# Performance work log

Hardware: AMD Instinct MI355X
Metric: run time of the kernel (lower is better)

## Reference

```python
import jax, jax.numpy as jnp
import numpy as np

SEQ, B, V, E, H, L, S_SRC = 128, 32, 32000, 1024, 1024, 3, 64


def setup_inputs() -> dict:
    key = jax.random.key(0)
    ks = jax.random.split(key, 8)
    sc = 0.05
    return {
        "tokens": jax.random.randint(ks[0], (SEQ, B), 0, V),
        "emb_W": jax.random.normal(ks[1], (V, E), jnp.float32) * 0.1,
        "W_ih": jax.random.normal(ks[2], (L, 4 * H, E), jnp.float32) * sc,
        "W_hh": jax.random.normal(ks[3], (L, 4 * H, H), jnp.float32) * sc,
        "b_ih": jnp.zeros((L, 4 * H), jnp.float32),
        "b_hh": jnp.zeros((L, 4 * H), jnp.float32),
        "attn_Win": jax.random.normal(ks[4], (E, E), jnp.float32) * sc,
        "attn_Wout": jax.random.normal(ks[5], (E, 2 * E), jnp.float32) * sc,
        "final_b": jnp.zeros((V,), jnp.float32),
        "encoder_outs": jax.random.normal(ks[6], (S_SRC, B, E), jnp.float32),
        "h0": jnp.zeros((L, B, H), jnp.float32),
        "c0": jnp.zeros((L, B, H), jnp.float32),
    }


def reference(tokens, emb_W, W_ih, W_hh, b_ih, b_hh, attn_Win, attn_Wout,
              final_b, encoder_outs, h0, c0):
    # Eval mode: all dropouts (dropoute/i/h/out) are identity.
    emb = emb_W[tokens]                                  # [SEQ, B, E]
    ctx = jnp.transpose(encoder_outs, (1, 0, 2))         # [B, S_src, E]

    def lstm_cell(x, h, c, l):
        gates = x @ W_ih[l].T + b_ih[l] + h @ W_hh[l].T + b_hh[l]  # [B, 4H]
        i, f, g, o = jnp.split(gates, 4, axis=-1)        # torch order: i,f,g,o
        i, f, o = jax.nn.sigmoid(i), jax.nn.sigmoid(f), jax.nn.sigmoid(o)
        g = jnp.tanh(g)
        c_new = f * c + i * g
        return o * jnp.tanh(c_new), c_new

    def step(carry, x_t):
        h, c = carry                                     # each [L, B, H]
        hs, cs = [], []
        inp = x_t
        for l in range(L):
            h_new, c_new = lstm_cell(inp, h[l], c[l], l)
            hs.append(h_new)
            cs.append(c_new)
            inp = h_new                                  # dropouth is identity
        # SoftDotAttention on last layer hidden
        target = h_new @ attn_Win.T                      # [B, E]
        attn = jax.nn.softmax(jnp.einsum('bse,be->bs', ctx, target), axis=-1)
        wc = jnp.einsum('bs,bse->be', attn, ctx)         # weighted context
        h_tilde = jnp.tanh(jnp.concatenate([wc, h_new], axis=-1) @ attn_Wout.T)
        return (jnp.stack(hs), jnp.stack(cs)), h_tilde

    (_, _), outs = jax.lax.scan(step, (h0, c0), emb)     # outs: [SEQ, B, E]
    logits = outs @ emb_W.T + final_b                    # tied weights: [SEQ, B, V]
    return logits
```

## Files before the change

### kernel.cpp

```cpp
#include <hip/hip_runtime.h>
#include <cstdint>
#include <cstddef>

#define SEQ   128
#define BB    32
#define EE    1024
#define HH    1024
#define G4    4096
#define VV    32000
#define NROWS 4096

typedef _Float16 h16x8 __attribute__((ext_vector_type(8)));
typedef _Float16 h16x4 __attribute__((ext_vector_type(4)));
typedef float f32x4  __attribute__((ext_vector_type(4)));

#define AS_G(p) ((const __attribute__((address_space(1))) void*)(p))
#define AS_L(p) ((__attribute__((address_space(3))) void*)(p))

__device__ __forceinline__ float sigmf(float x) { return 1.0f / (1.0f + expf(-x)); }

#define OFF_SYNC    0ull
#define OFF_HFRAG   40960ull
#define OFF_EMB     434176ull
#define OFF_X0      8822784ull
#define OFF_WIH0    42377216ull
#define OFF_WP4     50765824ull
#define OFF_WP0     84320256ull
#define OFF_EMBW    92708864ull
#define OFF_WIN     158244864ull
#define OFF_WOUT    160342016ull
#define OFF_ENC     164536320ull
#define OFF_H2ALL   168730624ull
#define OFF_CONCAT  177119232ull
#define OFF_TARGET  193896448ull
#define OFF_HT      202285056ull
#define WS_NEEDED   210673664ull

__global__ __launch_bounds__(256) void k_conv(const float* __restrict__ s,
                                              _Float16* __restrict__ d, int n4) {
  int i = blockIdx.x * blockDim.x + threadIdx.x;
  int st = gridDim.x * blockDim.x;
  for (; i < n4; i += st) {
    float4 v = ((const float4*)s)[i];
    h16x4 o; o[0] = (_Float16)v.x; o[1] = (_Float16)v.y; o[2] = (_Float16)v.z; o[3] = (_Float16)v.w;
    ((h16x4*)d)[i] = o;
  }
}

__global__ __launch_bounds__(256) void k_gather(const int* __restrict__ tok,
                                                const float* __restrict__ embW,
                                                _Float16* __restrict__ emb) {
  int row = blockIdx.x;
  int t = tok[row];
  float4 v = ((const float4*)(embW + (size_t)t * EE))[threadIdx.x];
  h16x4 o; o[0] = (_Float16)v.x; o[1] = (_Float16)v.y; o[2] = (_Float16)v.z; o[3] = (_Float16)v.w;
  ((h16x4*)(emb + (size_t)row * EE))[threadIdx.x] = o;
}

__global__ __launch_bounds__(256) void k_packw4(const float* __restrict__ Wih,
                                                const float* __restrict__ Whh,
                                                _Float16* __restrict__ out) {
  int i = blockIdx.x * blockDim.x + threadIdx.x;
  int st = gridDim.x * blockDim.x;
  const int total = 256 * 65536;
  for (; i < total; i += st) {
    int w = i >> 16, rem = i & 65535;
    int mat = rem >> 14, jj = (rem >> 10) & 15, k = rem & 1023;
    int layer = 1 + (mat >> 1), isHH = mat & 1;
    int row = ((jj >> 2) << 10) + (w << 2) + (jj & 3);
    int ks = k ^ ((jj & 7) << 3);
    const float* src = (isHH ? Whh : Wih) + (size_t)layer * G4 * 1024 + (size_t)row * 1024 + ks;
    out[i] = (_Float16)(*src);
  }
}

__global__ __launch_bounds__(256) void k_packw0(const float* __restrict__ Whh,
                                                _Float16* __restrict__ out) {
  int i = blockIdx.x * blockDim.x + threadIdx.x;
  int st = gridDim.x * blockDim.x;
  const int total = 256 * 16384;
  for (; i < total; i += st) {
    int w = i >> 14, rem = i & 16383;
    int ks = rem >> 9, lane = (rem >> 3) & 63, e = rem & 7;
    int jj = lane & 15, q = lane >> 4;
    int row = ((jj >> 2) << 10) + (w << 2) + (jj & 3);
    int k = ks * 32 + q * 8 + e;
    out[i] = (_Float16)Whh[(size_t)row * 1024 + k];
  }
}

__global__ __launch_bounds__(256) void k_init(const float* __restrict__ h0,
                                              _Float16* __restrict__ hfrag,
                                              unsigned* __restrict__ sync) {
  int i = blockIdx.x * blockDim.x + threadIdx.x;
  if (i < 64 + 8192) sync[i] = 0u;
  if (i >= 3 * BB * HH) return;
  int l = i >> 15, rem = i & 32767;
  int b = rem >> 10, n = rem & 1023;
  int parI = (l == 1) ? 0 : 1;
  int tbb = b >> 4, ks = n >> 5, q = (n >> 3) & 3, e = n & 7;
  int lane2 = (b & 15) | (q << 4);
  hfrag[(size_t)(l * 2 + parI) * 32768 + ((size_t)(tbb * 32 + ks) * 64 + lane2) * 8 + e] =
      (_Float16)h0[i];
}

template <int EPI>
__global__ __launch_bounds__(256) void k_gemm(const _Float16* __restrict__ A,
                                              const _Float16* __restrict__ B,
                                              void* __restrict__ C, int M, int N, int K,
                                              const float* __restrict__ bias1,
                                              const float* __restrict__ bias2) {
  __shared__ _Float16 As[2][128 * 32];
  __shared__ _Float16 Bs[2][128 * 32];
  const int ntn = N / 128;
  const int nwg = gridDim.x;
  const int bid = (blockIdx.x & 7) * (nwg >> 3) + (blockIdx.x >> 3);
  const int tm = bid / ntn, tn = bid % ntn;
  const int tid = threadIdx.x, lane = tid & 63;
  const int wv = tid >> 6, wr = wv >> 1, wc = wv & 1;
  f32x4 acc[4][4] = {};

  auto stage = [&](int buf, int k0) {
#pragma unroll
    for (int i = 0; i < 2; ++i) {
      int eo = (i * 256 + tid) * 8;
      int r = eo >> 5, c = eo & 31;
      __builtin_amdgcn_global_load_lds(AS_G(A + (size_t)(tm * 128 + r) * K + k0 + c),
                                       AS_L(&As[buf][eo]), 16, 0, 0);
      __builtin_amdgcn_global_load_lds(AS_G(B + (size_t)(tn * 128 + r) * K + k0 + c),
                                       AS_L(&Bs[buf][eo]), 16, 0, 0);
    }
  };
  stage(0, 0);
  __syncthreads();
  const int nk = K / 32;
  for (int kt = 0; kt < nk; ++kt) {
    if (kt + 1 < nk) stage((kt + 1) & 1, (kt + 1) * 32);
    const int buf = kt & 1;
    h16x8 af[4], bfr[4];
#pragma unroll
    for (int mi = 0; mi < 4; ++mi)
      af[mi] = *(const h16x8*)&As[buf][(wr * 64 + mi * 16 + (lane & 15)) * 32 + (lane >> 4) * 8];
#pragma unroll
    for (int ni = 0; ni < 4; ++ni)
      bfr[ni] = *(const h16x8*)&Bs[buf][(wc * 64 + ni * 16 + (lane & 15)) * 32 + (lane >> 4) * 8];
#pragma unroll
    for (int mi = 0; mi < 4; ++mi)
#pragma unroll
      for (int ni = 0; ni < 4; ++ni)
        acc[mi][ni] = __builtin_amdgcn_mfma_f32_16x16x32_f16(af[mi], bfr[ni], acc[mi][ni], 0, 0, 0);
    __syncthreads();
  }
  const int rbase = tm * 128 + wr * 64;
  const int cbase = tn * 128 + wc * 64;
#pragma unroll
  for (int mi = 0; mi < 4; ++mi) {
#pragma unroll
    for (int ni = 0; ni < 4; ++ni) {
#pragma unroll
      for (int r = 0; r < 4; ++r) {
        int mm = rbase + mi * 16 + (lane >> 4) * 4 + r;
        int nn = cbase + ni * 16 + (lane & 15);
        float v = acc[mi][ni][r];
        if (EPI == 0) {
          ((float*)C)[(size_t)mm * N + nn] = v + bias1[nn];
        } else if (EPI == 1) {
          ((_Float16*)C)[(size_t)mm * N + nn] = (_Float16)v;
        } else if (EPI == 2) {
          ((_Float16*)C)[(size_t)mm * N + nn] = (_Float16)tanhf(v);
        } else {
          ((_Float16*)C)[(size_t)mm * N + nn] = (_Float16)(v + bias1[nn] + bias2[nn]);
        }
      }
    }
  }
}

__global__ __launch_bounds__(512) void k_recur(const _Float16* __restrict__ Wp4,
                                               const _Float16* __restrict__ Wp0,
                                               const _Float16* __restrict__ X0bf,
                                               _Float16* __restrict__ hfrag,
                                               _Float16* __restrict__ h2all,
                                               _Float16* __restrict__ concat,
                                               const float* __restrict__ bih,
                                               const float* __restrict__ bhh,
                                               const float* __restrict__ c0p,
                                               unsigned* __restrict__ sync) {
  extern __shared__ char lds[];
  _Float16* ldsW = (_Float16*)lds;
  float* redbuf = (float*)(lds + 131072);
  _Float16* hstage = (_Float16*)(lds + 131072);
  float* gbuf = (float*)(lds + 149504);
  unsigned* arrive = sync + 64;

  const int w = blockIdx.x;
  const int tid = threadIdx.x, lane = tid & 63, wv = tid >> 6;
  const int tb = wv & 1, kq = wv >> 1;
  const int row = (lane >> 4) * 4, col = lane & 15;

  for (int i = 0; i < 16; ++i) {
    int eo = (i * 512 + tid) * 8;
    *(h16x8*)&ldsW[eo] = *(const h16x8*)(Wp4 + (size_t)w * 65536 + eo);
  }
  h16x8 w0reg[8];
#pragma unroll
  for (int i = 0; i < 8; ++i)
    w0reg[i] = *(const h16x8*)(Wp0 + (size_t)w * 16384 + ((size_t)(kq * 8 + i) * 64 + lane) * 8);

  const int eb = tid >> 2, eni = tid & 3, en = w * 4 + eni;
  float c0r = 0.f, c1r = 0.f, c2r = 0.f;
  float b1r[4] = {0, 0, 0, 0}, b2r[4] = {0, 0, 0, 0};
  if (tid < 128) {
    c0r = c0p[0 * BB * HH + eb * HH + en];
    c1r = c0p[1 * BB * HH + eb * HH + en];
    c2r = c0p[2 * BB * HH + eb * HH + en];
#pragma unroll
    for (int g = 0; g < 4; ++g) {
      b1r[g] = bih[1 * G4 + g * 1024 + en] + bhh[1 * G4 + g * 1024 + en];
      b2r[g] = bih[2 * G4 + g * 1024 + en] + bhh[2 * G4 + g * 1024 + en];
    }
  }
  const int pk_l = tid >> 5, pk_r = tid & 31;
  const size_t pk_idx = ((size_t)(((pk_r >> 4) * 32 + (w >> 3)) * 64 + (pk_r & 15) +
                                  (((w >> 1) & 3) << 4))) * 8 + 4 * (w & 1);
  __syncthreads();

  for (int tau = 0; tau < 130; ++tau) {
    const int p = tau & 1;
    const _Float16* h0r = hfrag + (size_t)(0 + (1 - p)) * 32768;
    const _Float16* h1r = hfrag + (size_t)(2 + (1 - p)) * 32768;
    const _Float16* h2r = hfrag + (size_t)(4 + (1 - p)) * 32768;

    h16x8 a0[8], a1[8], a2[8];
#pragma unroll
    for (int i = 0; i < 8; ++i) {
      int ks = kq * 8 + i;
      size_t off = ((size_t)(tb * 32 + ks) * 64 + lane) * 8;
      a0[i] = *(const h16x8*)(h0r + off);
      a1[i] = *(const h16x8*)(h1r + off);
      a2[i] = *(const h16x8*)(h2r + off);
    }
    float xg0 = 0.f, xg1 = 0.f, xg2 = 0.f, xg3 = 0.f;
    if (tid < 128 && tau < 128) {
      size_t xb = ((size_t)(tau * BB + eb)) * G4 + en;
      xg0 = (float)X0bf[xb];        xg1 = (float)X0bf[xb + 1024];
      xg2 = (float)X0bf[xb + 2048]; xg3 = (float)X0bf[xb + 3072];
    }
    f32x4 acc0 = {}, acc1 = {}, acc2 = {};
#pragma unroll
    for (int i = 0; i < 8; ++i) {
      int ks = kq * 8 + i;
      int jj = lane & 15, q = lane >> 4;
      int kk = (ks * 32 + q * 8) ^ ((jj & 7) << 3);
      const h16x8 bw1i = *(const h16x8*)&ldsW[0 * 16384 + jj * 1024 + kk];
      const h16x8 bw1h = *(const h16x8*)&ldsW[1 * 16384 + jj * 1024 + kk];
      const h16x8 bw2i = *(const h16x8*)&ldsW[2 * 16384 + jj * 1024 + kk];
      const h16x8 bw2h = *(const h16x8*)&ldsW[3 * 16384 + jj * 1024 + kk];
      acc0 = __builtin_amdgcn_mfma_f32_16x16x32_f16(a0[i], w0reg[i], acc0, 0, 0, 0);
      acc1 = __builtin_amdgcn_mfma_f32_16x16x32_f16(a0[i], bw1i, acc1, 0, 0, 0);
      acc1 = __builtin_amdgcn_mfma_f32_16x16x32_f16(a1[i], bw1h, acc1, 0, 0, 0);
      acc2 = __builtin_amdgcn_mfma_f32_16x16x32_f16(a1[i], bw2i, acc2, 0, 0, 0);
      acc2 = __builtin_amdgcn_mfma_f32_16x16x32_f16(a2[i], bw2h, acc2, 0, 0, 0);
    }
    if (kq >= 1) {
      int s = kq - 1;
#pragma unroll
      for (int r = 0; r < 4; ++r) {
        redbuf[((0 * 3 + s) * 2 + tb) * 256 + (row + r) * 16 + col] = acc0[r];
        redbuf[((1 * 3 + s) * 2 + tb) * 256 + (row + r) * 16 + col] = acc1[r];
        redbuf[((2 * 3 + s) * 2 + tb) * 256 + (row + r) * 16 + col] = acc2[r];
      }
    }
    __syncthreads();
    if (kq == 0) {
#pragma unroll
      for (int r = 0; r < 4; ++r) {
        float v0 = acc0[r], v1 = acc1[r], v2 = acc2[r];
#pragma unroll
        for (int s = 0; s < 3; ++s) {
          v0 += redbuf[((0 * 3 + s) * 2 + tb) * 256 + (row + r) * 16 + col];
          v1 += redbuf[((1 * 3 + s) * 2 + tb) * 256 + (row + r) * 16 + col];
          v2 += redbuf[((2 * 3 + s) * 2 + tb) * 256 + (row + r) * 16 + col];
        }
        gbuf[(0 * 32 + tb * 16 + row + r) * 16 + col] = v0;
        gbuf[(1 * 32 + tb * 16 + row + r) * 16 + col] = v1;
        gbuf[(2 * 32 + tb * 16 + row + r) * 16 + col] = v2;
      }
    }
    __syncthreads();
    if (tid < 128) {
      if (tau < 128) {
        float gi = gbuf[(0 * 32 + eb) * 16 + eni] + xg0;
        float gf = gbuf[(0 * 32 + eb) * 16 + 4 + eni] + xg1;
        float gg = gbuf[(0 * 32 + eb) * 16 + 8 + eni] + xg2;
        float go = gbuf[(0 * 32 + eb) * 16 + 12 + eni] + xg3;
        c0r = sigmf(gf) * c0r + sigmf(gi) * tanhf(gg);
        hstage[0 * 128 + tid] = (_Float16)(sigmf(go) * tanhf(c0r));
      }
      if (tau >= 1 && tau < 129) {
        float gi = gbuf[(1 * 32 + eb) * 16 + eni] + b1r[0];
        float gf = gbuf[(1 * 32 + eb) * 16 + 4 + eni] + b1r[1];
        float gg = gbuf[(1 * 32 + eb) * 16 + 8 + eni] + b1r[2];
        float go = gbuf[(1 * 32 + eb) * 16 + 12 + eni] + b1r[3];
        c1r = sigmf(gf) * c1r + sigmf(gi) * tanhf(gg);
        hstage[1 * 128 + tid] = (_Float16)(sigmf(go) * tanhf(c1r));
      }
      if (tau >= 2) {
        float gi = gbuf[(2 * 32 + eb) * 16 + eni] + b2r[0];
        float gf = gbuf[(2 * 32 + eb) * 16 + 4 + eni] + b2r[1];
        float gg = gbuf[(2 * 32 + eb) * 16 + 8 + eni] + b2r[2];
        float go = gbuf[(2 * 32 + eb) * 16 + 12 + eni] + b2r[3];
        c2r = sigmf(gf) * c2r + sigmf(gi) * tanhf(gg);
        float h = sigmf(go) * tanhf(c2r);
        _Float16 hb = (_Float16)h;
        hstage[2 * 128 + tid] = hb;
        int t2 = tau - 2;
        h2all[(size_t)(t2 * BB + eb) * HH + en] = hb;
        concat[(size_t)(t2 * BB + eb) * 2048 + 1024 + en] = hb;
      }
    }
    __syncthreads();
    {
      bool act = (tid < 96) &&
                 ((pk_l == 0) ? (tau < 128)
                  : (pk_l == 1) ? (tau >= 1 && tau < 129) : (tau >= 2));
      if (act) {
        unsigned long long v = *(const unsigned long long*)&hstage[pk_l * 128 + pk_r * 4];
        __hip_atomic_store(
            (unsigned long long*)(hfrag + (size_t)(pk_l * 2 + p) * 32768 + pk_idx), v,
            __ATOMIC_RELAXED, __HIP_MEMORY_SCOPE_AGENT);
      }
      asm volatile("s_waitcnt vmcnt(0)" ::: "memory");
    }
    __syncthreads();
    if (tid == 0)
      __hip_atomic_store(&arrive[w * 32], (unsigned)(tau + 1), __ATOMIC_RELAXED,
                         __HIP_MEMORY_SCOPE_AGENT);
    if (tau < 129) {
      if (tid < 64) {
        for (;;) {
          bool ok = true;
#pragma unroll
          for (int j = 0; j < 4; ++j) {
            unsigned v = __hip_atomic_load(&arrive[(tid * 4 + j) * 32], __ATOMIC_RELAXED,
                                           __HIP_MEMORY_SCOPE_AGENT);
            ok &= (v >= (unsigned)(tau + 1));
          }
          if (__all(ok)) break;
          __builtin_amdgcn_s_sleep(1);
        }
        __builtin_amdgcn_fence(__ATOMIC_ACQUIRE, "agent");
      }
      __syncthreads();
    }
  }
}

__global__ __launch_bounds__(256) void k_attn(const _Float16* __restrict__ target,
                                              const _Float16* __restrict__ encb,
                                              _Float16* __restrict__ concat) {
  __shared__ float sc[64];
  __shared__ float att[64];
  int m = blockIdx.x, b = m & 31;
  int tid = threadIdx.x, lane = tid & 63, wv = tid >> 6;
  const h16x8* tp = (const h16x8*)(target + (size_t)m * EE + lane * 16);
  h16x8 tg0 = tp[0], tg1 = tp[1];
  for (int si = 0; si < 16; ++si) {
    int s = wv * 16 + si;
    const h16x8* ep = (const h16x8*)(encb + ((size_t)s * BB + b) * EE + lane * 16);
    h16x8 e0 = ep[0], e1 = ep[1];
    float a = 0.f;
#pragma unroll
    for (int j = 0; j < 8; ++j) a += (float)e0[j] * (float)tg0[j];
#pragma unroll
    for (int j = 0; j < 8; ++j) a += (float)e1[j] * (float)tg1[j];
#pragma unroll
    for (int off = 32; off >= 1; off >>= 1) a += __shfl_xor(a, off);
    if (lane == 0) sc[s] = a;
  }
  __syncthreads();
  if (wv == 0) {
    float v = sc[lane], mx = v;
#pragma unroll
    for (int off = 32; off >= 1; off >>= 1) mx = fmaxf(mx, __shfl_xor(mx, off));
    float e = expf(v - mx), sm = e;
#pragma unroll
    for (int off = 32; off >= 1; off >>= 1) sm += __shfl_xor(sm, off);
    att[lane] = e / sm;
  }
  __syncthreads();
  int e4 = tid * 4;
  float a0 = 0, a1 = 0, a2 = 0, a3 = 0;
  for (int s = 0; s < 64; ++s) {
    float wgt = att[s];
    h16x4 ev = *(const h16x4*)(encb + ((size_t)s * BB + b) * EE + e4);
    a0 += wgt * (float)ev[0]; a1 += wgt * (float)ev[1];
    a2 += wgt * (float)ev[2]; a3 += wgt * (float)ev[3];
  }
  h16x4 o; o[0] = (_Float16)a0; o[1] = (_Float16)a1; o[2] = (_Float16)a2; o[3] = (_Float16)a3;
  *(h16x4*)(concat + (size_t)m * 2048 + e4) = o;
}

extern "C" void kernel_launch(void* const* d_in, const int* in_sizes, int n_in,
                              void* d_out, int out_size, void* d_ws, size_t ws_size,
                              hipStream_t stream) {
  const int* tokens = (const int*)d_in[0];
  const float* embW = (const float*)d_in[1];
  const float* Wih = (const float*)d_in[2];
  const float* Whh = (const float*)d_in[3];
  const float* bih = (const float*)d_in[4];
  const float* bhh = (const float*)d_in[5];
  const float* Win = (const float*)d_in[6];
  const float* Wout = (const float*)d_in[7];
  const float* finalb = (const float*)d_in[8];
  const float* enc = (const float*)d_in[9];
  const float* h0 = (const float*)d_in[10];
  const float* c0 = (const float*)d_in[11];
  (void)in_sizes; (void)n_in; (void)out_size;
  if (ws_size < WS_NEEDED) return;

  char* ws = (char*)d_ws;
  unsigned* sync = (unsigned*)(ws + OFF_SYNC);
  _Float16* hfrag = (_Float16*)(ws + OFF_HFRAG);
  _Float16* emb = (_Float16*)(ws + OFF_EMB);
  _Float16* X0bf = (_Float16*)(ws + OFF_X0);
  _Float16* Wih0b = (_Float16*)(ws + OFF_WIH0);
  _Float16* Wp4 = (_Float16*)(ws + OFF_WP4);
  _Float16* Wp0 = (_Float16*)(ws + OFF_WP0);
  _Float16* embWb = (_Float16*)(ws + OFF_EMBW);
  _Float16* Winb = (_Float16*)(ws + OFF_WIN);
  _Float16* Woutb = (_Float16*)(ws + OFF_WOUT);
  _Float16* encb = (_Float16*)(ws + OFF_ENC);
  _Float16* h2all = (_Float16*)(ws + OFF_H2ALL);
  _Float16* concat = (_Float16*)(ws + OFF_CONCAT);
  _Float16* target = (_Float16*)(ws + OFF_TARGET);
  _Float16* ht = (_Float16*)(ws + OFF_HT);

  const unsigned LDSB = 155648;
  static int lds_set = 0;
  if (!lds_set) {
    hipFuncSetAttribute((const void*)k_recur, hipFuncAttributeMaxDynamicSharedMemorySize,
                        (int)LDSB);
    lds_set = 1;
  }

  k_conv<<<4096, 256, 0, stream>>>(embW, embWb, VV * EE / 4);
  k_conv<<<1024, 256, 0, stream>>>(Wih, Wih0b, G4 * EE / 4);
  k_conv<<<512, 256, 0, stream>>>(Win, Winb, EE * EE / 4);
  k_conv<<<512, 256, 0, stream>>>(Wout, Woutb, EE * 2048 / 4);
  k_conv<<<512, 256, 0, stream>>>(enc, encb, 64 * BB * EE / 4);
  k_gather<<<NROWS, 256, 0, stream>>>(tokens, embW, emb);
  k_packw4<<<8192, 256, 0, stream>>>(Wih, Whh, Wp4);
  k_packw0<<<4096, 256, 0, stream>>>(Whh, Wp0);
  k_init<<<384, 256, 0, stream>>>(h0, hfrag, sync);

  k_gemm<3><<<32 * 32, 256, 0, stream>>>(emb, Wih0b, X0bf, NROWS, G4, EE, bih, bhh);

  k_recur<<<256, 512, LDSB, stream>>>(Wp4, Wp0, X0bf, hfrag, h2all, concat,
                                      bih, bhh, c0, sync);

  k_gemm<1><<<32 * 8, 256, 0, stream>>>(h2all, Winb, target, NROWS, EE, EE, nullptr, nullptr);
  k_attn<<<NROWS, 256, 0, stream>>>(target, encb, concat);
  k_gemm<2><<<32 * 8, 256, 0, stream>>>(concat, Woutb, ht, NROWS, EE, 2048, nullptr, nullptr);

  k_gemm<0><<<32 * 250, 256, 0, stream>>>(ht, embWb, d_out, NROWS, VV, EE, finalb, nullptr);
}
```

Before: 1.697 ms.

## Add 256x256-tile triple-buffered GEMM for input projection and vocab logits

Adds a new GEMM kernel with 256x256 output tiles, 512 threads, three-stage global-to-LDS async loads and wave priority boosting around the MFMA block. It is used for the layer-0 input projection and the large tied-embedding logits GEMM, replacing the 128x128 kernel, to raise data reuse per loaded tile and overlap loads with compute. The old kernel keeps only the fp16 and tanh epilogues. The new kernel uses more registers and LDS per workgroup, so occupancy is lower. It also adds a blockIdx remap across groups of eight.

```diff
diff --git a/kernel.cpp b/kernel.cpp
--- a/kernel.cpp
+++ b/kernel.cpp
@@ -162,12 +162,100 @@
         int mm = rbase + mi * 16 + (lane >> 4) * 4 + r;
         int nn = cbase + ni * 16 + (lane & 15);
         float v = acc[mi][ni][r];
+        if (EPI == 1) {
+          ((_Float16*)C)[(size_t)mm * N + nn] = (_Float16)v;
+        } else {
+          ((_Float16*)C)[(size_t)mm * N + nn] = (_Float16)tanhf(v);
+        }
+      }
+    }
+  }
+}
+
+template <int EPI>
+__global__ __launch_bounds__(512, 2) void k_gemm256(const _Float16* __restrict__ A,
+                                                    const _Float16* __restrict__ B,
+                                                    void* __restrict__ C, int M, int N, int K,
+                                                    const float* __restrict__ bias1,
+                                                    const float* __restrict__ bias2) {
+  extern __shared__ char glds[];
+  _Float16* Asl = (_Float16*)glds;
+  _Float16* Bsl = (_Float16*)(glds + 3 * 8192 * 2);
+  const int ntn = N / 256;
+  const int nwg = gridDim.x;
+  const int bid = (blockIdx.x & 7) * (nwg >> 3) + (blockIdx.x >> 3);
+  const int tm = bid / ntn, tn = bid % ntn;
+  const int tid = threadIdx.x, lane = tid & 63;
+  const int wid = tid >> 6, wm = wid >> 2, wn = wid & 3;
+  const int fr = lane & 15, fc = lane >> 4;
+  const int srow0 = tid >> 2, sg = tid & 3;
+
+  f32x4 acc[8][4] = {};
+  const int nt = K / 32;
+
+  auto stage = [&](int t) {
+    const int slot = t % 3;
+    const size_t kof = (size_t)t * 32 + sg * 8;
+#pragma unroll
+    for (int r = 0; r < 2; ++r) {
+      int row = r * 128 + srow0;
+      __builtin_amdgcn_global_load_lds(AS_G(A + (size_t)(tm * 256 + row) * K + kof),
+                                       AS_L(&Asl[slot * 8192 + row * 32 + sg * 8]), 16, 0, 0);
+    }
+#pragma unroll
+    for (int r = 0; r < 2; ++r) {
+      int row = r * 128 + srow0;
+      __builtin_amdgcn_global_load_lds(AS_G(B + (size_t)(tn * 256 + row) * K + kof),
+                                       AS_L(&Bsl[slot * 8192 + row * 32 + sg * 8]), 16, 0, 0);
+    }
+  };
+
+  stage(0);
+  stage(1);
+  asm volatile("s_waitcnt vmcnt(4)" ::: "memory");
+  asm volatile("s_barrier" ::: "memory");
+
+  for (int t = 0; t < nt; ++t) {
+    if (t + 2 < nt) {
+      stage(t + 2);
+      asm volatile("s_waitcnt vmcnt(4)" ::: "memory");
+    } else {
+      asm volatile("s_waitcnt vmcnt(0)" ::: "memory");
+    }
+    asm volatile("s_barrier" ::: "memory");
+    const int slot = t % 3;
+    const _Float16* as = &Asl[slot * 8192];
+    const _Float16* bs = &Bsl[slot * 8192];
+    h16x8 af[8], bf[4];
+#pragma unroll
+    for (int mi = 0; mi < 8; ++mi)
+      af[mi] = *(const h16x8*)&as[(wm * 128 + mi * 16 + fr) * 32 + fc * 8];
+#pragma unroll
+    for (int ni = 0; ni < 4; ++ni)
+      bf[ni] = *(const h16x8*)&bs[(wn * 64 + ni * 16 + fr) * 32 + fc * 8];
+    __builtin_amdgcn_s_setprio(1);
+#pragma unroll
+    for (int mi = 0; mi < 8; ++mi)
+#pragma unroll
+      for (int ni = 0; ni < 4; ++ni)
+        acc[mi][ni] = __builtin_amdgcn_mfma_f32_16x16x32_f16(af[mi], bf[ni], acc[mi][ni], 0, 0, 0);
+    __builtin_amdgcn_s_setprio(0);
+    asm volatile("s_barrier" ::: "memory");
+  }
+
+  const int rbase = tm * 256 + wm * 128;
+  const int cbase = tn * 256 + wn * 64;
+#pragma unroll
+  for (int mi = 0; mi < 8; ++mi) {
+#pragma unroll
+    for (int ni = 0; ni < 4; ++ni) {
+#pragma unroll
+      for (int r = 0; r < 4; ++r) {
+        int mm = rbase + mi * 16 + fc * 4 + r;
+        int nn = cbase + ni * 16 + fr;
+        float v = acc[mi][ni][r];
         if (EPI == 0) {
           ((float*)C)[(size_t)mm * N + nn] = v + bias1[nn];
-        } else if (EPI == 1) {
-          ((_Float16*)C)[(size_t)mm * N + nn] = (_Float16)v;
-        } else if (EPI == 2) {
-          ((_Float16*)C)[(size_t)mm * N + nn] = (_Float16)tanhf(v);
         } else {
           ((_Float16*)C)[(size_t)mm * N + nn] = (_Float16)(v + bias1[nn] + bias2[nn]);
         }
@@ -437,10 +525,15 @@
   _Float16* ht = (_Float16*)(ws + OFF_HT);
 
   const unsigned LDSB = 155648;
+  const unsigned LDSG = 98304;
   static int lds_set = 0;
   if (!lds_set) {
     hipFuncSetAttribute((const void*)k_recur, hipFuncAttributeMaxDynamicSharedMemorySize,
                         (int)LDSB);
+    hipFuncSetAttribute((const void*)k_gemm256<0>, hipFuncAttributeMaxDynamicSharedMemorySize,
+                        (int)LDSG);
+    hipFuncSetAttribute((const void*)k_gemm256<1>, hipFuncAttributeMaxDynamicSharedMemorySize,
+                        (int)LDSG);
     lds_set = 1;
   }
 
@@ -454,7 +547,7 @@
   k_packw0<<<4096, 256, 0, stream>>>(Whh, Wp0);
   k_init<<<384, 256, 0, stream>>>(h0, hfrag, sync);
 
-  k_gemm<3><<<32 * 32, 256, 0, stream>>>(emb, Wih0b, X0bf, NROWS, G4, EE, bih, bhh);
+  k_gemm256<1><<<16 * 16, 512, LDSG, stream>>>(emb, Wih0b, X0bf, NROWS, G4, EE, bih, bhh);
 
   k_recur<<<256, 512, LDSB, stream>>>(Wp4, Wp0, X0bf, hfrag, h2all, concat,
                                       bih, bhh, c0, sync);
@@ -463,5 +556,5 @@
   k_attn<<<NROWS, 256, 0, stream>>>(target, encb, concat);
   k_gemm<2><<<32 * 8, 256, 0, stream>>>(concat, Woutb, ht, NROWS, EE, 2048, nullptr, nullptr);
 
-  k_gemm<0><<<32 * 250, 256, 0, stream>>>(ht, embWb, d_out, NROWS, VV, EE, finalb, nullptr);
-}
+  k_gemm256<0><<<16 * 125, 512, LDSG, stream>>>(ht, embWb, d_out, NROWS, VV, EE, finalb, nullptr);
+}
```

New measurement: 1.637 ms. -3.6%, faster.
